# Kernel optimization log

Measured on AMD Instinct MI355X. Metric: run time of the kernel, lower is better.

The kernel has to match this reference:

```python
import jax, jax.numpy as jnp
import numpy as np

B, P, T, C, S = 4, 4, 16, 32, 96  # batch, patch, ntime, nlatent, nspatial


def setup_inputs() -> dict:
    key = jax.random.key(0)
    k0, k1, k2, k3 = jax.random.split(key, 4)
    # xavier_uniform for a 3D tensor [S, S, C]: fan_in = S*C, fan_out = S*C
    bound = float(np.sqrt(6.0 / (S * C + S * C)))
    Q = jax.random.uniform(k0, (S, S, C), minval=-bound, maxval=bound, dtype=jnp.float32)
    K = jax.random.uniform(k1, (S, S, C), minval=-bound, maxval=bound, dtype=jnp.float32)
    V = jax.random.uniform(k2, (S, S, C), minval=-bound, maxval=bound, dtype=jnp.float32)
    Aoo = jnp.full((S, S, T), 1.0 / T, dtype=jnp.float32)
    w = jnp.ones((S,), dtype=jnp.float32) / S
    x = jax.random.normal(k3, (B, P, T, C, S), dtype=jnp.float32)
    return {"x": x, "Q": Q, "K": K, "V": V, "Aoo": Aoo, "w": w}


def reference(x, Q, K, V, Aoo, w):
    # kvt[B,p,T,X,Y] = sum_{x,c} Q[Y,x,c] K[X,x,c] x[B,p,T,c,x]
    # minimal-FLOP path: pre-combine Q and K (elementwise over x,c), then contract.
    QK = jnp.einsum('Yxc,Xxc->XYxc', Q, K)          # [S,S,S,C]
    kvt = jnp.einsum('XYxc,BpTcx->BpTXY', QK, x)     # [B,P,T,S,S]
    # time mixing with Aoo
    h = jnp.einsum('xXT,BpTxX->BpxX', Aoo, kvt)      # [B,P,S,S]
    # V applied to the last time step
    q = jnp.einsum('Xxc,Bpcx->BpcX', V, x[:, :, -1]) # [B,P,C,S]
    # w-weighted combine
    y = jnp.einsum('x,BpcX,BpXx->Bpc', w, q, h)      # [B,P,C]
    return y[:, :, None, :]                          # [B,P,1,C]
```

## Files before the change

kernel.cpp:

```cpp
#include <hip/hip_runtime.h>

#define SS 96
#define CC 32
#define TT 16
#define BP 16
#define MM 3072
#define KTOT 49152
#define NKB 96

typedef float f32x4 __attribute__((ext_vector_type(4)));
typedef short short8 __attribute__((ext_vector_type(8)));

__device__ __forceinline__ unsigned short f2b(float f) {
    union { float f; unsigned u; } a; a.f = f;
    unsigned r = a.u + 0x7FFFu + ((a.u >> 16) & 1u);
    return (unsigned short)(r >> 16);
}


__global__ __launch_bounds__(256) void k_prep(
    const float* __restrict__ x, const float* __restrict__ Q,
    const float* __restrict__ K, const float* __restrict__ V,
    const float* __restrict__ Aoo, const float* __restrict__ w,
    float* __restrict__ Kt, unsigned short* __restrict__ Qbf,
    unsigned short* __restrict__ wabf, unsigned short* __restrict__ xbf,
    float* __restrict__ q)
{
    __shared__ __align__(16) union {
        float sb[SS * 33];
        unsigned short cvt[16][520];
    } sm;
    const int bid = blockIdx.x, tid = threadIdx.x;
    if (bid < 96) {
        const int X = bid;
        const float* src = K + (size_t)X * MM;
        float* dst = Kt + (size_t)X * MM;
        for (int i = tid; i < MM; i += 256) {
            int e = i >> 5, c = i & 31;
            sm.sb[e * 33 + c] = src[i];
        }
        __syncthreads();
        for (int j = tid; j < MM; j += 256) {
            int c = j / SS, e = j - c * SS;
            dst[j] = sm.sb[e * 33 + c];
        }
    } else if (bid < 192) {
        const int e = bid - 96;
        for (int i = tid; i < MM; i += 256) {
            int v = i >> 5, c = i & 31;
            sm.sb[v * 33 + c] = Q[(size_t)v * MM + e * 32 + c];
        }
        __syncthreads();
        for (int g = tid; g < 384; g += 256) {
            const int c = g / 12, vg = g - c * 12;
            const int mtile = c * 6 + (e >> 4);
            const int kt = vg >> 2;
            const int lane = ((vg & 3) << 4) | (e & 15);
            short8 o;
#pragma unroll
            for (int j = 0; j < 8; ++j)
                o[j] = (short)f2b(sm.sb[(vg * 8 + j) * 33 + c]);
            *(short8*)(Qbf + (size_t)(mtile * 3 + kt) * 512 + lane * 8) = o;
        }
    } else if (bid < 288) {
        const int X = bid - 192;
        for (int i = tid; i < SS * TT; i += 256)
            sm.sb[i] = Aoo[(size_t)X * (SS * TT) + i];
        if (tid < SS) sm.sb[1600 + tid] = w[tid];
        __syncthreads();
        if (tid < 192) {
            const int kt = tid >> 6, l = tid & 63;
            const int t = l & 15, v0 = kt * 32 + ((l >> 4) << 3);
            short8 o;
#pragma unroll
            for (int j = 0; j < 8; ++j)
                o[j] = (short)f2b(sm.sb[1600 + v0 + j] * sm.sb[(v0 + j) * 16 + t]);
            *(short8*)(wabf + (size_t)(X * 3 + kt) * 512 + l * 8) = o;
        }
    } else if (bid < 384) {
        const int cb = bid - 288;
        const int b = tid >> 4, cb32 = (tid & 15) * 32;
        const float* xp = x + (size_t)b * KTOT + cb * 512 + cb32;
#pragma unroll
        for (int k = 0; k < 32; k += 4) {
            float4 v4 = *(const float4*)(xp + k);
            sm.cvt[b][cb32 + k + 0] = f2b(v4.x);
            sm.cvt[b][cb32 + k + 1] = f2b(v4.y);
            sm.cvt[b][cb32 + k + 2] = f2b(v4.z);
            sm.cvt[b][cb32 + k + 3] = f2b(v4.w);
        }
        __syncthreads();
#pragma unroll
        for (int it = 0; it < 4; ++it) {
            const int i = tid + it * 256;
            const int kt2 = i >> 6, l = i & 63;
            short8 o = *(const short8*)(&sm.cvt[l & 15][kt2 * 32 + ((l >> 4) << 3)]);
            *(short8*)(xbf + ((size_t)(cb * 16 + kt2) * 64 + l) * 8) = o;
        }
    } else {
        const int qb = bid - 384;
        const int bp = qb / 12, xc = qb - (qb / 12) * 12;
        const float* xs = x + (size_t)bp * (TT * MM) + (TT - 1) * MM;
        for (int i = tid; i < MM; i += 256) {
            int c = i / SS, e = i - (i / SS) * SS;
            sm.sb[e * 33 + c] = xs[i];
        }
        __syncthreads();
        const int c = tid & 31, grp = tid >> 5;
        const int X = xc * 8 + grp;
        const float* Vp = V + (size_t)X * MM + c;
        float acc = 0.f;
#pragma unroll 8
        for (int e = 0; e < SS; ++e)
            acc = fmaf(Vp[e * CC], sm.sb[e * 33 + c], acc);
        q[((size_t)bp * SS + X) * CC + c] = acc;
    }
}

__global__ __launch_bounds__(256) void k_fused(
    const unsigned short* __restrict__ Qbf, const unsigned short* __restrict__ wabf,
    const float* __restrict__ Kt, const unsigned short* __restrict__ xbf,
    float* __restrict__ Gp)
{
    __shared__ __align__(16) unsigned short w2s[16 * 516];
    __shared__ float red[1024];
    const int flat = blockIdx.x;
    const int bid = (flat & 7) * 72 + (flat >> 3);
    const int mc = bid / 6, xt = bid - (bid / 6) * 6;
    const int tid = threadIdx.x;
    const int lane = tid & 63, wv = tid >> 6;
    const int l15 = lane & 15, lg = lane >> 4;

    short8 af[2][3];
#pragma unroll
    for (int mtl = 0; mtl < 2; ++mtl)
#pragma unroll
        for (int kt = 0; kt < 3; ++kt)
            af[mtl][kt] = *(const short8*)(
                Qbf + (size_t)((mc * 2 + mtl) * 3 + kt) * 512 + lane * 8);

#pragma unroll
    for (int xi = 0; xi < 4; ++xi) {
        const int Xl = wv * 4 + xi;
        const int X = xt * 16 + Xl;
        const unsigned short* bw = wabf + (size_t)X * 3 * 512 + lane * 8;
        const short8 b0 = *(const short8*)(bw);
        const short8 b1 = *(const short8*)(bw + 512);
        const short8 b2 = *(const short8*)(bw + 1024);
#pragma unroll
        for (int mtl = 0; mtl < 2; ++mtl) {
            f32x4 acc = {0.f, 0.f, 0.f, 0.f};
            acc = __builtin_amdgcn_mfma_f32_16x16x32_bf16(af[mtl][0], b0, acc, 0, 0, 0);
            acc = __builtin_amdgcn_mfma_f32_16x16x32_bf16(af[mtl][1], b1, acc, 0, 0, 0);
            acc = __builtin_amdgcn_mfma_f32_16x16x32_bf16(af[mtl][2], b2, acc, 0, 0, 0);
            const int mloc = mtl * 16 + lg * 4;
            const f32x4 kt4 = *(const f32x4*)(Kt + (size_t)X * MM + mc * 32 + mloc);
            ushort4 o;
            o.x = f2b(acc[0] * kt4[0]);
            o.y = f2b(acc[1] * kt4[1]);
            o.z = f2b(acc[2] * kt4[2]);
            o.w = f2b(acc[3] * kt4[3]);
            *(ushort4*)(&w2s[l15 * 516 + ((mloc >> 3) * 16 + Xl) * 8 + (lg & 1) * 4]) = o;
        }
    }
    __syncthreads();

    f32x4 acc2 = {0.f, 0.f, 0.f, 0.f};
#pragma unroll
    for (int ts = 0; ts < 4; ++ts) {
        const int t = wv * 4 + ts;
        const short8 a2 = *(const short8*)(&w2s[t * 516 + lane * 8]);
        const short8 b2f = *(const short8*)(xbf + ((size_t)(t * SS + mc) * 64 + lane) * 8);
        acc2 = __builtin_amdgcn_mfma_f32_16x16x32_bf16(a2, b2f, acc2, 0, 0, 0);
    }
#pragma unroll
    for (int r = 0; r < 4; ++r)
        red[(wv * 64 + lane) * 4 + r] = acc2[r];
    __syncthreads();
    {
        const int Xl = tid >> 4, b = tid & 15;
        const int l = ((Xl >> 2) << 4) | b, r = Xl & 3;
        float s = red[(0 * 64 + l) * 4 + r] + red[(1 * 64 + l) * 4 + r] +
                  red[(2 * 64 + l) * 4 + r] + red[(3 * 64 + l) * 4 + r];
        Gp[(size_t)((xt * 16 + Xl) * BP + b) * NKB + mc] = s;
    }
}

__global__ __launch_bounds__(256) void k_final(
    const float* __restrict__ Gp, const float* __restrict__ q,
    float* __restrict__ y)
{
    const int bp = blockIdx.x, tid = threadIdx.x;
    __shared__ float Gh[SS][2];
    __shared__ float G[SS];
    __shared__ float red2[8 * CC];
    if (tid < 192) {
        const int X = tid >> 1, h = tid & 1;
        const float* p = Gp + (size_t)(X * BP + bp) * NKB + h * 48;
        float s = 0.f;
#pragma unroll
        for (int j = 0; j < 12; ++j) {
            f32x4 v4 = *(const f32x4*)(p + j * 4);
            s += v4[0] + v4[1] + v4[2] + v4[3];
        }
        Gh[X][h] = s;
    }
    __syncthreads();
    if (tid < SS) G[tid] = Gh[tid][0] + Gh[tid][1];
    __syncthreads();

    const int c = tid & 31, grp = tid >> 5;
    float acc = 0.f;
#pragma unroll
    for (int k = 0; k < 12; ++k) {
        const int X = grp * 12 + k;
        acc = fmaf(q[((size_t)bp * SS + X) * CC + c], G[X], acc);
    }
    red2[grp * CC + c] = acc;
    __syncthreads();
    if (tid < CC) {
        float s = 0.f;
#pragma unroll
        for (int g8 = 0; g8 < 8; ++g8) s += red2[g8 * CC + tid];
        y[bp * CC + tid] = s;
    }
}

extern "C" void kernel_launch(void* const* d_in, const int* in_sizes, int n_in,
                              void* d_out, int out_size, void* d_ws, size_t ws_size,
                              hipStream_t stream) {
    const float* x   = (const float*)d_in[0];
    const float* Q   = (const float*)d_in[1];
    const float* K   = (const float*)d_in[2];
    const float* V   = (const float*)d_in[3];
    const float* Aoo = (const float*)d_in[4];
    const float* w   = (const float*)d_in[5];

    char* wsb = (char*)d_ws;
    float*          Kt   = (float*)(wsb);
    float*          Gp   = (float*)(wsb + 1179648);
    float*          qb_  = (float*)(wsb + 1769472);
    unsigned short* Qbf  = (unsigned short*)(wsb + 1966080);
    unsigned short* wabf = (unsigned short*)(wsb + 2555904);
    unsigned short* xbf  = (unsigned short*)(wsb + 2850816);
    float* y = (float*)d_out;

    k_prep<<<dim3(576), 256, 0, stream>>>(x, Q, K, V, Aoo, w, Kt, Qbf, wabf,
                                          xbf, qb_);
    k_fused<<<dim3(576), 256, 0, stream>>>(Qbf, wabf, Kt, xbf, Gp);
    k_final<<<dim3(BP), 256, 0, stream>>>(Gp, qb_, y);
}
```

Before: 20.07 us.

## Fuse final reduction into main kernel via atomicAdd, drop k_final launch

Removes the third kernel and the Gp partial buffer. Each fused block now contracts its local G tile against q and atomically adds its contribution into y, which the prep kernel zeroes first. This saves one launch, the Gp round trip and the launch gap. In exchange it adds 576 blocks times 512 atomics onto only 512 addresses, which may contend, and it makes the summation order nondeterministic.

```diff
diff --git a/kernel.cpp b/kernel.cpp
--- a/kernel.cpp
+++ b/kernel.cpp
@@ -6,7 +6,6 @@
 #define BP 16
 #define MM 3072
 #define KTOT 49152
-#define NKB 96
 
 typedef float f32x4 __attribute__((ext_vector_type(4)));
 typedef short short8 __attribute__((ext_vector_type(8)));
@@ -24,13 +23,14 @@
     const float* __restrict__ Aoo, const float* __restrict__ w,
     float* __restrict__ Kt, unsigned short* __restrict__ Qbf,
     unsigned short* __restrict__ wabf, unsigned short* __restrict__ xbf,
-    float* __restrict__ q)
+    float* __restrict__ q, float* __restrict__ y)
 {
     __shared__ __align__(16) union {
         float sb[SS * 33];
         unsigned short cvt[16][520];
     } sm;
     const int bid = blockIdx.x, tid = threadIdx.x;
+    if (bid == 0) { y[tid] = 0.f; y[tid + 256] = 0.f; }
     if (bid < 96) {
         const int X = bid;
         const float* src = K + (size_t)X * MM;
@@ -120,10 +120,11 @@
 __global__ __launch_bounds__(256) void k_fused(
     const unsigned short* __restrict__ Qbf, const unsigned short* __restrict__ wabf,
     const float* __restrict__ Kt, const unsigned short* __restrict__ xbf,
-    float* __restrict__ Gp)
+    const float* __restrict__ q, float* __restrict__ y)
 {
     __shared__ __align__(16) unsigned short w2s[16 * 516];
     __shared__ float red[1024];
+    __shared__ float Gloc[256];
     const int flat = blockIdx.x;
     const int bid = (flat & 7) * 72 + (flat >> 3);
     const int mc = bid / 6, xt = bid - (bid / 6) * 6;
@@ -180,49 +181,21 @@
     {
         const int Xl = tid >> 4, b = tid & 15;
         const int l = ((Xl >> 2) << 4) | b, r = Xl & 3;
-        float s = red[(0 * 64 + l) * 4 + r] + red[(1 * 64 + l) * 4 + r] +
-                  red[(2 * 64 + l) * 4 + r] + red[(3 * 64 + l) * 4 + r];
-        Gp[(size_t)((xt * 16 + Xl) * BP + b) * NKB + mc] = s;
-    }
-}
-
-__global__ __launch_bounds__(256) void k_final(
-    const float* __restrict__ Gp, const float* __restrict__ q,
-    float* __restrict__ y)
-{
-    const int bp = blockIdx.x, tid = threadIdx.x;
-    __shared__ float Gh[SS][2];
-    __shared__ float G[SS];
-    __shared__ float red2[8 * CC];
-    if (tid < 192) {
-        const int X = tid >> 1, h = tid & 1;
-        const float* p = Gp + (size_t)(X * BP + bp) * NKB + h * 48;
-        float s = 0.f;
-#pragma unroll
-        for (int j = 0; j < 12; ++j) {
-            f32x4 v4 = *(const f32x4*)(p + j * 4);
-            s += v4[0] + v4[1] + v4[2] + v4[3];
-        }
-        Gh[X][h] = s;
+        Gloc[tid] = red[(0 * 64 + l) * 4 + r] + red[(1 * 64 + l) * 4 + r] +
+                    red[(2 * 64 + l) * 4 + r] + red[(3 * 64 + l) * 4 + r];
     }
     __syncthreads();
-    if (tid < SS) G[tid] = Gh[tid][0] + Gh[tid][1];
-    __syncthreads();
-
-    const int c = tid & 31, grp = tid >> 5;
-    float acc = 0.f;
-#pragma unroll
-    for (int k = 0; k < 12; ++k) {
-        const int X = grp * 12 + k;
-        acc = fmaf(q[((size_t)bp * SS + X) * CC + c], G[X], acc);
-    }
-    red2[grp * CC + c] = acc;
-    __syncthreads();
-    if (tid < CC) {
-        float s = 0.f;
-#pragma unroll
-        for (int g8 = 0; g8 < 8; ++g8) s += red2[g8 * CC + tid];
-        y[bp * CC + tid] = s;
+
+#pragma unroll
+    for (int pass = 0; pass < 2; ++pass) {
+        const int out = tid + pass * 256;
+        const int bp = out >> 5, c = out & 31;
+        const float* qp = q + ((size_t)bp * SS + xt * 16) * CC + c;
+        float a = 0.f;
+#pragma unroll
+        for (int Xl = 0; Xl < 16; ++Xl)
+            a = fmaf(qp[(size_t)Xl * CC], Gloc[Xl * BP + bp], a);
+        atomicAdd(&y[out], a);
     }
 }
 
@@ -238,15 +211,13 @@
 
     char* wsb = (char*)d_ws;
     float*          Kt   = (float*)(wsb);
-    float*          Gp   = (float*)(wsb + 1179648);
-    float*          qb_  = (float*)(wsb + 1769472);
-    unsigned short* Qbf  = (unsigned short*)(wsb + 1966080);
-    unsigned short* wabf = (unsigned short*)(wsb + 2555904);
-    unsigned short* xbf  = (unsigned short*)(wsb + 2850816);
+    float*          qb_  = (float*)(wsb + 1179648);
+    unsigned short* Qbf  = (unsigned short*)(wsb + 1376256);
+    unsigned short* wabf = (unsigned short*)(wsb + 1966080);
+    unsigned short* xbf  = (unsigned short*)(wsb + 2260992);
     float* y = (float*)d_out;
 
     k_prep<<<dim3(576), 256, 0, stream>>>(x, Q, K, V, Aoo, w, Kt, Qbf, wabf,
-                                          xbf, qb_);
-    k_fused<<<dim3(576), 256, 0, stream>>>(Qbf, wabf, Kt, xbf, Gp);
-    k_final<<<dim3(BP), 256, 0, stream>>>(Gp, qb_, y);
-}
+                                          xbf, qb_, y);
+    k_fused<<<dim3(576), 256, 0, stream>>>(Qbf, wabf, Kt, xbf, qb_, y);
+}
```

Result: slower. 31.24 us (+55.7%).

## Drop K transpose, reorder Q/x bf16 tiling, move V projection into fused kernel

Applied to the files above, without the earlier changes.

Remaps the reduction index ordering so the MFMA M dimension follows K's native (x,c) layout, which removes the separate K-transpose pass and its workspace buffer. The Q and x bf16 packing is rewritten to match the new index order, and the x packing is regrouped per time step and spatial block. The V-projection blocks move from the prep kernel into the fused kernel as extra blocks that share a shared-memory union. Prep work and launch size shrink, at the cost of the fused kernel carrying a heterogeneous block mix and a new, untested index mapping.

```diff
diff --git a/kernel.cpp b/kernel.cpp
--- a/kernel.cpp
+++ b/kernel.cpp
@@ -20,32 +20,17 @@
 
 __global__ __launch_bounds__(256) void k_prep(
     const float* __restrict__ x, const float* __restrict__ Q,
-    const float* __restrict__ K, const float* __restrict__ V,
     const float* __restrict__ Aoo, const float* __restrict__ w,
-    float* __restrict__ Kt, unsigned short* __restrict__ Qbf,
-    unsigned short* __restrict__ wabf, unsigned short* __restrict__ xbf,
-    float* __restrict__ q)
+    unsigned short* __restrict__ Qbf, unsigned short* __restrict__ wabf,
+    unsigned short* __restrict__ xbf)
 {
     __shared__ __align__(16) union {
         float sb[SS * 33];
-        unsigned short cvt[16][520];
+        unsigned short cv[16][16][40];
     } sm;
     const int bid = blockIdx.x, tid = threadIdx.x;
     if (bid < 96) {
-        const int X = bid;
-        const float* src = K + (size_t)X * MM;
-        float* dst = Kt + (size_t)X * MM;
-        for (int i = tid; i < MM; i += 256) {
-            int e = i >> 5, c = i & 31;
-            sm.sb[e * 33 + c] = src[i];
-        }
-        __syncthreads();
-        for (int j = tid; j < MM; j += 256) {
-            int c = j / SS, e = j - c * SS;
-            dst[j] = sm.sb[e * 33 + c];
-        }
-    } else if (bid < 192) {
-        const int e = bid - 96;
+        const int e = bid;
         for (int i = tid; i < MM; i += 256) {
             int v = i >> 5, c = i & 31;
             sm.sb[v * 33 + c] = Q[(size_t)v * MM + e * 32 + c];
@@ -53,17 +38,17 @@
         __syncthreads();
         for (int g = tid; g < 384; g += 256) {
             const int c = g / 12, vg = g - c * 12;
-            const int mtile = c * 6 + (e >> 4);
+            const int mtile = e * 2 + (c >> 4);
             const int kt = vg >> 2;
-            const int lane = ((vg & 3) << 4) | (e & 15);
+            const int lane = ((vg & 3) << 4) | (c & 15);
             short8 o;
 #pragma unroll
             for (int j = 0; j < 8; ++j)
-                o[j] = (short)f2b(sm.sb[(vg * 8 + j) * 33 + c]);
+                o[j] = (short)f2b(sm.sb[(kt * 32 + (vg & 3) * 8 + j) * 33 + c]);
             *(short8*)(Qbf + (size_t)(mtile * 3 + kt) * 512 + lane * 8) = o;
         }
-    } else if (bid < 288) {
-        const int X = bid - 192;
+    } else if (bid < 192) {
+        const int X = bid - 96;
         for (int i = tid; i < SS * TT; i += 256)
             sm.sb[i] = Aoo[(size_t)X * (SS * TT) + i];
         if (tid < SS) sm.sb[1600 + tid] = w[tid];
@@ -77,33 +62,59 @@
                 o[j] = (short)f2b(sm.sb[1600 + v0 + j] * sm.sb[(v0 + j) * 16 + t]);
             *(short8*)(wabf + (size_t)(X * 3 + kt) * 512 + l * 8) = o;
         }
-    } else if (bid < 384) {
-        const int cb = bid - 288;
-        const int b = tid >> 4, cb32 = (tid & 15) * 32;
-        const float* xp = x + (size_t)b * KTOT + cb * 512 + cb32;
-#pragma unroll
-        for (int k = 0; k < 32; k += 4) {
-            float4 v4 = *(const float4*)(xp + k);
-            sm.cvt[b][cb32 + k + 0] = f2b(v4.x);
-            sm.cvt[b][cb32 + k + 1] = f2b(v4.y);
-            sm.cvt[b][cb32 + k + 2] = f2b(v4.z);
-            sm.cvt[b][cb32 + k + 3] = f2b(v4.w);
+    } else {
+        const int cb = bid - 192;
+        const int t = cb / 6, eg = cb - (cb / 6) * 6;
+        const int e0 = eg * 16;
+#pragma unroll
+        for (int it = 0; it < 2; ++it) {
+            const int p = it * 256 + tid;
+            const int b = p >> 5, c = p & 31;
+            const float* xp = x + (size_t)b * KTOT + (size_t)t * MM + c * SS + e0;
+#pragma unroll
+            for (int k = 0; k < 16; k += 4) {
+                float4 v4 = *(const float4*)(xp + k);
+                sm.cv[b][k + 0][c] = f2b(v4.x);
+                sm.cv[b][k + 1][c] = f2b(v4.y);
+                sm.cv[b][k + 2][c] = f2b(v4.z);
+                sm.cv[b][k + 3][c] = f2b(v4.w);
+            }
         }
         __syncthreads();
 #pragma unroll
         for (int it = 0; it < 4; ++it) {
-            const int i = tid + it * 256;
-            const int kt2 = i >> 6, l = i & 63;
-            short8 o = *(const short8*)(&sm.cvt[l & 15][kt2 * 32 + ((l >> 4) << 3)]);
-            *(short8*)(xbf + ((size_t)(cb * 16 + kt2) * 64 + l) * 8) = o;
-        }
-    } else {
-        const int qb = bid - 384;
+            const int slot = it * 256 + tid;
+            const int tileL = slot >> 6, l = slot & 63;
+            short8 o = *(const short8*)(&sm.cv[l & 15][tileL][(l >> 4) * 8]);
+            *(short8*)(xbf + ((size_t)(t * SS + e0 + tileL) * 64 + l) * 8) = o;
+        }
+    }
+}
+
+__global__ __launch_bounds__(256) void k_fused(
+    const unsigned short* __restrict__ Qbf, const unsigned short* __restrict__ wabf,
+    const float* __restrict__ K, const unsigned short* __restrict__ xbf,
+    const float* __restrict__ x, const float* __restrict__ V,
+    float* __restrict__ Gp, float* __restrict__ q)
+{
+    __shared__ __align__(16) union {
+        struct {
+            unsigned short w2s[16 * 516];
+            float red[1024];
+            float Gloc[256];
+        } g;
+        float qsm[SS * 33];
+    } sm;
+    const int flat = blockIdx.x;
+    const int tid = threadIdx.x;
+
+    if (flat >= 576) {
+        const int qb = flat - 576;
         const int bp = qb / 12, xc = qb - (qb / 12) * 12;
         const float* xs = x + (size_t)bp * (TT * MM) + (TT - 1) * MM;
         for (int i = tid; i < MM; i += 256) {
             int c = i / SS, e = i - (i / SS) * SS;
-            sm.sb[e * 33 + c] = xs[i];
+            sm.qsm[e * 33 + c] = xs[i];
         }
         __syncthreads();
         const int c = tid & 31, grp = tid >> 5;
@@ -112,22 +123,12 @@
         float acc = 0.f;
 #pragma unroll 8
         for (int e = 0; e < SS; ++e)
-            acc = fmaf(Vp[e * CC], sm.sb[e * 33 + c], acc);
+            acc = fmaf(Vp[e * CC], sm.qsm[e * 33 + c], acc);
         q[((size_t)bp * SS + X) * CC + c] = acc;
-    }
-}
-
-__global__ __launch_bounds__(256) void k_fused(
-    const unsigned short* __restrict__ Qbf, const unsigned short* __restrict__ wabf,
-    const float* __restrict__ Kt, const unsigned short* __restrict__ xbf,
-    float* __restrict__ Gp)
-{
-    __shared__ __align__(16) unsigned short w2s[16 * 516];
-    __shared__ float red[1024];
-    const int flat = blockIdx.x;
+        return;
+    }
     const int bid = (flat & 7) * 72 + (flat >> 3);
     const int mc = bid / 6, xt = bid - (bid / 6) * 6;
-    const int tid = threadIdx.x;
     const int lane = tid & 63, wv = tid >> 6;
     const int l15 = lane & 15, lg = lane >> 4;
 
@@ -154,13 +155,13 @@
             acc = __builtin_amdgcn_mfma_f32_16x16x32_bf16(af[mtl][1], b1, acc, 0, 0, 0);
             acc = __builtin_amdgcn_mfma_f32_16x16x32_bf16(af[mtl][2], b2, acc, 0, 0, 0);
             const int mloc = mtl * 16 + lg * 4;
-            const f32x4 kt4 = *(const f32x4*)(Kt + (size_t)X * MM + mc * 32 + mloc);
+            const f32x4 kt4 = *(const f32x4*)(K + (size_t)X * MM + mc * 32 + mloc);
             ushort4 o;
             o.x = f2b(acc[0] * kt4[0]);
             o.y = f2b(acc[1] * kt4[1]);
             o.z = f2b(acc[2] * kt4[2]);
             o.w = f2b(acc[3] * kt4[3]);
-            *(ushort4*)(&w2s[l15 * 516 + ((mloc >> 3) * 16 + Xl) * 8 + (lg & 1) * 4]) = o;
+            *(ushort4*)(&sm.g.w2s[l15 * 516 + ((mloc >> 3) * 16 + Xl) * 8 + (lg & 1) * 4]) = o;
         }
     }
     __syncthreads();
@@ -169,19 +170,19 @@
 #pragma unroll
     for (int ts = 0; ts < 4; ++ts) {
         const int t = wv * 4 + ts;
-        const short8 a2 = *(const short8*)(&w2s[t * 516 + lane * 8]);
+        const short8 a2 = *(const short8*)(&sm.g.w2s[t * 516 + lane * 8]);
         const short8 b2f = *(const short8*)(xbf + ((size_t)(t * SS + mc) * 64 + lane) * 8);
         acc2 = __builtin_amdgcn_mfma_f32_16x16x32_bf16(a2, b2f, acc2, 0, 0, 0);
     }
 #pragma unroll
     for (int r = 0; r < 4; ++r)
-        red[(wv * 64 + lane) * 4 + r] = acc2[r];
+        sm.g.red[(wv * 64 + lane) * 4 + r] = acc2[r];
     __syncthreads();
     {
         const int Xl = tid >> 4, b = tid & 15;
         const int l = ((Xl >> 2) << 4) | b, r = Xl & 3;
-        float s = red[(0 * 64 + l) * 4 + r] + red[(1 * 64 + l) * 4 + r] +
-                  red[(2 * 64 + l) * 4 + r] + red[(3 * 64 + l) * 4 + r];
+        float s = sm.g.red[(0 * 64 + l) * 4 + r] + sm.g.red[(1 * 64 + l) * 4 + r] +
+                  sm.g.red[(2 * 64 + l) * 4 + r] + sm.g.red[(3 * 64 + l) * 4 + r];
         Gp[(size_t)((xt * 16 + Xl) * BP + b) * NKB + mc] = s;
     }
 }
@@ -237,16 +238,14 @@
     const float* w   = (const float*)d_in[5];
 
     char* wsb = (char*)d_ws;
-    float*          Kt   = (float*)(wsb);
-    float*          Gp   = (float*)(wsb + 1179648);
-    float*          qb_  = (float*)(wsb + 1769472);
-    unsigned short* Qbf  = (unsigned short*)(wsb + 1966080);
-    unsigned short* wabf = (unsigned short*)(wsb + 2555904);
-    unsigned short* xbf  = (unsigned short*)(wsb + 2850816);
+    float*          Gp   = (float*)(wsb);
+    float*          qb_  = (float*)(wsb + 589824);
+    unsigned short* Qbf  = (unsigned short*)(wsb + 786432);
+    unsigned short* wabf = (unsigned short*)(wsb + 1376256);
+    unsigned short* xbf  = (unsigned short*)(wsb + 1671168);
     float* y = (float*)d_out;
 
-    k_prep<<<dim3(576), 256, 0, stream>>>(x, Q, K, V, Aoo, w, Kt, Qbf, wabf,
-                                          xbf, qb_);
-    k_fused<<<dim3(576), 256, 0, stream>>>(Qbf, wabf, Kt, xbf, Gp);
+    k_prep<<<dim3(288), 256, 0, stream>>>(x, Q, Aoo, w, Qbf, wabf, xbf);
+    k_fused<<<dim3(768), 256, 0, stream>>>(Qbf, wabf, K, xbf, x, V, Gp, qb_);
     k_final<<<dim3(BP), 256, 0, stream>>>(Gp, qb_, y);
 }
```

Measured after the change: 20.37 us. Within noise of the previous version (+1.5%).
